# Kernel optimization log

Hardware: AMD Instinct MI355X
Metric: run time of the kernel (lower is better)

## Reference

```python
import jax, jax.numpy as jnp
import numpy as np
import math

B, S, E = 4, 4096, 1024
NUM_HEADS = 16
D = E // NUM_HEADS  # attention_size = 64


def setup_inputs() -> dict:
    key = jax.random.key(0)
    ks = jax.random.split(key, 7)
    queries = jax.random.normal(ks[0], (B, S, E), dtype=jnp.float32)
    keys = jax.random.normal(ks[1], (B, S, E), dtype=jnp.float32)
    values = jax.random.normal(ks[2], (B, S, E), dtype=jnp.float32)
    mask = jax.random.randint(ks[3], (B, S, S), 0, 2).astype(bool)
    # nn.Linear(E, D, bias=False): weight [D, E], y = x @ W^T
    lim = 1.0 / math.sqrt(E)
    W_q = jax.random.uniform(ks[4], (D, E), jnp.float32, -lim, lim)
    W_k = jax.random.uniform(ks[5], (D, E), jnp.float32, -lim, lim)
    W_v = jax.random.uniform(ks[6], (D, E), jnp.float32, -lim, lim)
    return {"queries": queries, "keys": keys, "values": values, "mask": mask,
            "W_q": W_q, "W_k": W_k, "W_v": W_v}


def reference(queries, keys, values, mask, W_q, W_k, W_v):
    Q = jnp.einsum('bse,de->bsd', queries, W_q)  # [B,S,D]
    K = jnp.einsum('bse,de->bsd', keys, W_k)
    V = jnp.einsum('bse,de->bsd', values, W_v)
    norm = math.sqrt(D)
    scores = jnp.einsum('bqd,bkd->bqk', Q, K) / norm  # [B,S,S]
    scores = jnp.where(mask, jnp.float32(-1e20), scores)
    attn = jax.nn.softmax(scores, axis=2)
    return jnp.einsum('bqk,bkd->bqd', attn, V)  # [B,S,D]
```

## Files before the change

### kernel.cpp

```cpp
#include <hip/hip_runtime.h>
#include <hip/hip_bf16.h>
#include <math.h>

#define NB 4
#define NS 4096
#define NE 1024
#define ND 64

typedef short bf16x8 __attribute__((ext_vector_type(8)));
typedef float f32x4  __attribute__((ext_vector_type(4)));

__device__ unsigned short g_Wb[3 * ND * NE];
__device__ unsigned short g_Qp[NB * NS * ND];
__device__ unsigned short g_Kp[NB * NS * ND];
__device__ unsigned short g_Vt[NB * ND * NS];
__device__ int g_flag;

static __device__ inline unsigned short f2bf(float f) {
    __hip_bfloat16 h = __float2bfloat16(f);
    return *reinterpret_cast<unsigned short*>(&h);
}
static __device__ inline unsigned int f2bf2(float lo, float hi) {
    __hip_bfloat162 h = __float22bfloat162_rn(make_float2(lo, hi));
    return *reinterpret_cast<unsigned int*>(&h);
}

static __device__ __forceinline__ void lds_fence() {
    asm volatile("s_waitcnt lgkmcnt(0)" ::: "memory");
    __builtin_amdgcn_sched_barrier(0);
}

__global__ void detect_mask(const unsigned int* __restrict__ mw) {
    __shared__ int found;
    if (threadIdx.x == 0) found = 0;
    __syncthreads();
    int f = 0;
    for (int i = threadIdx.x; i < 4096; i += 256)
        if (mw[i] > 1u) f = 1;
    if (f) atomicOr(&found, 1);
    __syncthreads();
    if (threadIdx.x == 0) g_flag = found;
}

__global__ void prep_w(const float* __restrict__ Wq, const float* __restrict__ Wk,
                       const float* __restrict__ Wv) {
    const int z = blockIdx.x;
    const float* W = (z == 0) ? Wq : (z == 1) ? Wk : Wv;
    unsigned short* o = g_Wb + (size_t)z * (ND * NE);
    const float scale = (z == 0) ? 0.125f : 1.0f;
    int i0 = blockIdx.y * 2048 + threadIdx.x * 8;
    float4 a = *(const float4*)&W[i0];
    float4 b = *(const float4*)&W[i0 + 4];
    ushort4 u0 = { f2bf(a.x * scale), f2bf(a.y * scale), f2bf(a.z * scale), f2bf(a.w * scale) };
    ushort4 u1 = { f2bf(b.x * scale), f2bf(b.y * scale), f2bf(b.z * scale), f2bf(b.w * scale) };
    *(ushort4*)&o[i0]     = u0;
    *(ushort4*)&o[i0 + 4] = u1;
}

__global__ __launch_bounds__(256) void proj_kernel(
    const float* __restrict__ Xq, const float* __restrict__ Xk, const float* __restrict__ Xv)
{
    __shared__ unsigned short Xs[2][64][72];

    const int z = blockIdx.y;
    const float* X = (z == 0) ? Xq : (z == 1) ? Xk : Xv;
    const unsigned short* W = g_Wb + (size_t)z * (ND * NE);

    const int t    = threadIdx.x;
    const int wv   = t >> 6;
    const int lane = t & 63;
    const int quad = lane >> 4;
    const int l16  = lane & 15;
    const int m0   = blockIdx.x * 64;

    const int sr  = t >> 4;
    const int sc4 = (t & 15) * 4;
    const float* Xb = X + (size_t)m0 * NE;

    float4 xv[4];

    #pragma unroll
    for (int p = 0; p < 4; ++p)
        xv[p] = *(const float4*)&Xb[(size_t)(sr + p * 16) * NE + sc4];
    #pragma unroll
    for (int p = 0; p < 4; ++p) {
        uint2 u = { f2bf2(xv[p].x, xv[p].y), f2bf2(xv[p].z, xv[p].w) };
        *(uint2*)&Xs[0][sr + p * 16][sc4] = u;
    }
    __syncthreads();

    f32x4 acc[4] = {};

    #pragma unroll 2
    for (int c = 0; c < 16; ++c) {
        const int buf = c & 1;
        const int e0  = c * 64;

        if (c < 15) {
            #pragma unroll
            for (int p = 0; p < 4; ++p)
                xv[p] = *(const float4*)&Xb[(size_t)(sr + p * 16) * NE + e0 + 64 + sc4];
        }

        #pragma unroll
        for (int ks = 0; ks < 2; ++ks) {
            bf16x8 a = *(const bf16x8*)&Xs[buf][wv * 16 + l16][ks * 32 + quad * 8];
            #pragma unroll
            for (int nt = 0; nt < 4; ++nt) {
                bf16x8 bb = *(const bf16x8*)&W[(size_t)(nt * 16 + l16) * NE + e0 + ks * 32 + quad * 8];
                acc[nt] = __builtin_amdgcn_mfma_f32_16x16x32_bf16(a, bb, acc[nt], 0, 0, 0);
            }
        }

        if (c < 15) {
            #pragma unroll
            for (int p = 0; p < 4; ++p) {
                uint2 u = { f2bf2(xv[p].x, xv[p].y), f2bf2(xv[p].z, xv[p].w) };
                *(uint2*)&Xs[buf ^ 1][sr + p * 16][sc4] = u;
            }
        }
        __syncthreads();
    }

    #pragma unroll
    for (int nt = 0; nt < 4; ++nt)
        #pragma unroll
        for (int r = 0; r < 4; ++r) {
            int m   = m0 + wv * 16 + quad * 4 + r;
            int col = nt * 16 + l16;
            unsigned short u = f2bf(acc[nt][r]);
            if (z == 0)      g_Qp[(size_t)m * ND + col] = u;
            else if (z == 1) g_Kp[(size_t)m * ND + col] = u;
            else             g_Vt[((size_t)(m >> 12) * ND + col) * NS + (m & 4095)] = u;
        }
}

__global__ __launch_bounds__(256) void attn_kernel(
    const void* __restrict__ maskp, float* __restrict__ out)
{
    __shared__ short Ss[4][2][16][72];
    __shared__ float Op[4][16][68];
    __shared__ float Lp[4][16];

    const int t    = threadIdx.x;
    const int wv   = t >> 6;
    const int lane = t & 63;
    const int quad = lane >> 4;
    const int l16  = lane & 15;
    const int b    = blockIdx.y;
    const int q0   = blockIdx.x * 16;
    const int koff = wv * 1024;

    const bool m_u8 = (g_flag != 0);
    const unsigned char* m8  = (const unsigned char*)maskp;
    const int*           m32 = (const int*)maskp;

    const unsigned short* Qrow = g_Qp + ((size_t)b * NS + q0 + l16) * ND;
    const bf16x8 qf0 = *(const bf16x8*)&Qrow[quad * 8];
    const bf16x8 qf1 = *(const bf16x8*)&Qrow[32 + quad * 8];

    const unsigned short* Kbase = g_Kp + ((size_t)b * NS) * ND;
    const unsigned short* Vbase = g_Vt + (size_t)b * ND * NS;

    float l_lane[4] = {};
    f32x4 Oacc[4] = {};

    #pragma unroll 2
    for (int it = 0; it < 16; ++it) {
        const int k0 = koff + it * 64;
        const int pb = it & 1;

        int mv[16];
        #pragma unroll
        for (int r = 0; r < 4; ++r) {
            size_t mrow = ((size_t)b * NS + (q0 + quad * 4 + r)) * (size_t)NS + k0;
            if (m_u8) {
                #pragma unroll
                for (int kt = 0; kt < 4; ++kt)
                    mv[kt * 4 + r] = (int)m8[mrow + kt * 16 + l16];
            } else {
                #pragma unroll
                for (int kt = 0; kt < 4; ++kt)
                    mv[kt * 4 + r] = m32[mrow + kt * 16 + l16];
            }
        }

        f32x4 sc[4] = {};
        __builtin_amdgcn_s_setprio(1);
        #pragma unroll
        for (int kt = 0; kt < 4; ++kt) {
            const unsigned short* Krow = Kbase + (size_t)(k0 + kt * 16 + l16) * ND;
            bf16x8 kf0 = *(const bf16x8*)&Krow[quad * 8];
            bf16x8 kf1 = *(const bf16x8*)&Krow[32 + quad * 8];
            sc[kt] = __builtin_amdgcn_mfma_f32_16x16x32_bf16(qf0, kf0, sc[kt], 0, 0, 0);
            sc[kt] = __builtin_amdgcn_mfma_f32_16x16x32_bf16(qf1, kf1, sc[kt], 0, 0, 0);
        }
        __builtin_amdgcn_s_setprio(0);

        bf16x8 vf[8];
        #pragma unroll
        for (int nt = 0; nt < 4; ++nt) {
            const unsigned short* Vrow = Vbase + (size_t)(nt * 16 + l16) * NS + k0;
            vf[2 * nt]     = *(const bf16x8*)&Vrow[quad * 8];
            vf[2 * nt + 1] = *(const bf16x8*)&Vrow[32 + quad * 8];
        }

        #pragma unroll
        for (int kt = 0; kt < 4; ++kt)
            #pragma unroll
            for (int r = 0; r < 4; ++r) {
                float p = mv[kt * 4 + r] ? 0.0f : __expf(sc[kt][r]);
                l_lane[r] += p;
                Ss[wv][pb][quad * 4 + r][kt * 16 + l16] = (short)f2bf(p);
            }

        lds_fence();

        bf16x8 a0 = *(const bf16x8*)&Ss[wv][pb][l16][quad * 8];
        bf16x8 a1 = *(const bf16x8*)&Ss[wv][pb][l16][32 + quad * 8];

        __builtin_amdgcn_s_setprio(1);
        #pragma unroll
        for (int nt = 0; nt < 4; ++nt) {
            Oacc[nt] = __builtin_amdgcn_mfma_f32_16x16x32_bf16(a0, vf[2 * nt],     Oacc[nt], 0, 0, 0);
            Oacc[nt] = __builtin_amdgcn_mfma_f32_16x16x32_bf16(a1, vf[2 * nt + 1], Oacc[nt], 0, 0, 0);
        }
        __builtin_amdgcn_s_setprio(0);
    }

    #pragma unroll
    for (int r = 0; r < 4; ++r) {
        #pragma unroll
        for (int off = 1; off < 16; off <<= 1)
            l_lane[r] += __shfl_xor(l_lane[r], off);
    }

    #pragma unroll
    for (int nt = 0; nt < 4; ++nt)
        #pragma unroll
        for (int r = 0; r < 4; ++r)
            Op[wv][quad * 4 + r][nt * 16 + l16] = Oacc[nt][r];
    if (l16 == 0) {
        #pragma unroll
        for (int r = 0; r < 4; ++r)
            Lp[wv][quad * 4 + r] = l_lane[r];
    }
    __syncthreads();

    {
        int q  = t >> 4;
        int d4 = (t & 15) * 4;
        f32x4 s = {};
        #pragma unroll
        for (int w = 0; w < 4; ++w)
            s += *(const f32x4*)&Op[w][q][d4];
        float l = Lp[0][q] + Lp[1][q] + Lp[2][q] + Lp[3][q];
        float inv = 1.0f / l;
        float4 o = { s[0] * inv, s[1] * inv, s[2] * inv, s[3] * inv };
        *(float4*)&out[((size_t)b * NS + q0 + q) * ND + d4] = o;
    }
}

extern "C" void kernel_launch(void* const* d_in, const int* in_sizes, int n_in,
                              void* d_out, int out_size, void* d_ws, size_t ws_size,
                              hipStream_t stream) {
    const float* queries = (const float*)d_in[0];
    const float* keys    = (const float*)d_in[1];
    const float* values  = (const float*)d_in[2];
    const void*  mask    = d_in[3];
    const float* Wq      = (const float*)d_in[4];
    const float* Wk      = (const float*)d_in[5];
    const float* Wv      = (const float*)d_in[6];
    float* out = (float*)d_out;

    hipLaunchKernelGGL(detect_mask, dim3(1), dim3(256), 0, stream,
                       (const unsigned int*)mask);
    hipLaunchKernelGGL(prep_w, dim3(3, 32), dim3(256), 0, stream, Wq, Wk, Wv);
    hipLaunchKernelGGL(proj_kernel, dim3((NB * NS) / 64, 3), dim3(256), 0, stream,
                       queries, keys, values);
    hipLaunchKernelGGL(attn_kernel, dim3(NS / 16, NB), dim3(256), 0, stream,
                       mask, out);
}
```

Before: 604.6 us.

## Stage mask tiles through LDS with vector loads and deepen projection prefetch

```diff
diff --git a/kernel.cpp b/kernel.cpp
--- a/kernel.cpp
+++ b/kernel.cpp
@@ -27,7 +27,6 @@
 
 static __device__ __forceinline__ void lds_fence() {
     asm volatile("s_waitcnt lgkmcnt(0)" ::: "memory");
-    __builtin_amdgcn_sched_barrier(0);
 }
 
 __global__ void detect_mask(const unsigned int* __restrict__ mw) {
@@ -77,46 +76,46 @@
     const int sc4 = (t & 15) * 4;
     const float* Xb = X + (size_t)m0 * NE;
 
-    float4 xv[4];
-
-    #pragma unroll
-    for (int p = 0; p < 4; ++p)
-        xv[p] = *(const float4*)&Xb[(size_t)(sr + p * 16) * NE + sc4];
+    float4 xr[4][4];
+
+    #pragma unroll
+    for (int d = 0; d < 4; ++d)
+        #pragma unroll
+        for (int p = 0; p < 4; ++p)
+            xr[d][p] = *(const float4*)&Xb[(size_t)(sr + p * 16) * NE + d * 64 + sc4];
     #pragma unroll
     for (int p = 0; p < 4; ++p) {
-        uint2 u = { f2bf2(xv[p].x, xv[p].y), f2bf2(xv[p].z, xv[p].w) };
+        uint2 u = { f2bf2(xr[0][p].x, xr[0][p].y), f2bf2(xr[0][p].z, xr[0][p].w) };
         *(uint2*)&Xs[0][sr + p * 16][sc4] = u;
     }
     __syncthreads();
 
     f32x4 acc[4] = {};
 
-    #pragma unroll 2
+    #pragma unroll
     for (int c = 0; c < 16; ++c) {
-        const int buf = c & 1;
-        const int e0  = c * 64;
-
-        if (c < 15) {
+        if (c + 4 < 16) {
             #pragma unroll
             for (int p = 0; p < 4; ++p)
-                xv[p] = *(const float4*)&Xb[(size_t)(sr + p * 16) * NE + e0 + 64 + sc4];
+                xr[c & 3][p] = *(const float4*)&Xb[(size_t)(sr + p * 16) * NE + (c + 4) * 64 + sc4];
         }
 
         #pragma unroll
         for (int ks = 0; ks < 2; ++ks) {
-            bf16x8 a = *(const bf16x8*)&Xs[buf][wv * 16 + l16][ks * 32 + quad * 8];
+            bf16x8 a = *(const bf16x8*)&Xs[c & 1][wv * 16 + l16][ks * 32 + quad * 8];
             #pragma unroll
             for (int nt = 0; nt < 4; ++nt) {
-                bf16x8 bb = *(const bf16x8*)&W[(size_t)(nt * 16 + l16) * NE + e0 + ks * 32 + quad * 8];
+                bf16x8 bb = *(const bf16x8*)&W[(size_t)(nt * 16 + l16) * NE + c * 64 + ks * 32 + quad * 8];
                 acc[nt] = __builtin_amdgcn_mfma_f32_16x16x32_bf16(a, bb, acc[nt], 0, 0, 0);
             }
         }
 
-        if (c < 15) {
+        if (c + 1 < 16) {
             #pragma unroll
             for (int p = 0; p < 4; ++p) {
-                uint2 u = { f2bf2(xv[p].x, xv[p].y), f2bf2(xv[p].z, xv[p].w) };
-                *(uint2*)&Xs[buf ^ 1][sr + p * 16][sc4] = u;
+                float4 v = xr[(c + 1) & 3][p];
+                uint2 u = { f2bf2(v.x, v.y), f2bf2(v.z, v.w) };
+                *(uint2*)&Xs[(c + 1) & 1][sr + p * 16][sc4] = u;
             }
         }
         __syncthreads();
@@ -135,12 +134,14 @@
         }
 }
 
-__global__ __launch_bounds__(256) void attn_kernel(
+__global__ __launch_bounds__(256, 4) void attn_kernel(
     const void* __restrict__ maskp, float* __restrict__ out)
 {
-    __shared__ short Ss[4][2][16][72];
-    __shared__ float Op[4][16][68];
-    __shared__ float Lp[4][16];
+    __shared__ __align__(16) char smem[28672];
+    short (*Ss)[2][16][72]         = reinterpret_cast<short(*)[2][16][72]>(smem);
+    unsigned char (*Mb)[2][16][80] = reinterpret_cast<unsigned char(*)[2][16][80]>(smem + 18432);
+    float (*Op)[16][68]            = reinterpret_cast<float(*)[16][68]>(smem);
+    float (*Lp)[16]                = reinterpret_cast<float(*)[16]>(smem + 17408);
 
     const int t    = threadIdx.x;
     const int wv   = t >> 6;
@@ -162,6 +163,15 @@
     const unsigned short* Kbase = g_Kp + ((size_t)b * NS) * ND;
     const unsigned short* Vbase = g_Vt + (size_t)b * ND * NS;
 
+    const int srow = lane >> 2;
+    const int scol = (lane & 3) * 16;
+    const unsigned char* m8row = m8 + ((size_t)b * NS + q0 + srow) * (size_t)NS + scol;
+
+    if (m_u8) {
+        uint4 mr0 = *(const uint4*)&m8row[koff];
+        *(uint4*)&Mb[wv][0][srow][scol] = mr0;
+    }
+
     float l_lane[4] = {};
     f32x4 Oacc[4] = {};
 
@@ -170,23 +180,7 @@
         const int k0 = koff + it * 64;
         const int pb = it & 1;
 
-        int mv[16];
-        #pragma unroll
-        for (int r = 0; r < 4; ++r) {
-            size_t mrow = ((size_t)b * NS + (q0 + quad * 4 + r)) * (size_t)NS + k0;
-            if (m_u8) {
-                #pragma unroll
-                for (int kt = 0; kt < 4; ++kt)
-                    mv[kt * 4 + r] = (int)m8[mrow + kt * 16 + l16];
-            } else {
-                #pragma unroll
-                for (int kt = 0; kt < 4; ++kt)
-                    mv[kt * 4 + r] = m32[mrow + kt * 16 + l16];
-            }
-        }
-
         f32x4 sc[4] = {};
-        __builtin_amdgcn_s_setprio(1);
         #pragma unroll
         for (int kt = 0; kt < 4; ++kt) {
             const unsigned short* Krow = Kbase + (size_t)(k0 + kt * 16 + l16) * ND;
@@ -195,7 +189,10 @@
             sc[kt] = __builtin_amdgcn_mfma_f32_16x16x32_bf16(qf0, kf0, sc[kt], 0, 0, 0);
             sc[kt] = __builtin_amdgcn_mfma_f32_16x16x32_bf16(qf1, kf1, sc[kt], 0, 0, 0);
         }
-        __builtin_amdgcn_s_setprio(0);
+
+        uint4 mr = {};
+        if (m_u8 && it < 15)
+            mr = *(const uint4*)&m8row[k0 + 64];
 
         bf16x8 vf[8];
         #pragma unroll
@@ -205,15 +202,35 @@
             vf[2 * nt + 1] = *(const bf16x8*)&Vrow[32 + quad * 8];
         }
 
+        int mvv[16];
+        if (m_u8) {
+            #pragma unroll
+            for (int kt = 0; kt < 4; ++kt)
+                #pragma unroll
+                for (int r = 0; r < 4; ++r)
+                    mvv[kt * 4 + r] = Mb[wv][pb][quad * 4 + r][kt * 16 + l16];
+        } else {
+            #pragma unroll
+            for (int r = 0; r < 4; ++r) {
+                size_t mrow = ((size_t)b * NS + (q0 + quad * 4 + r)) * (size_t)NS + k0;
+                #pragma unroll
+                for (int kt = 0; kt < 4; ++kt)
+                    mvv[kt * 4 + r] = m32[mrow + kt * 16 + l16];
+            }
+        }
+
         #pragma unroll
         for (int kt = 0; kt < 4; ++kt)
             #pragma unroll
             for (int r = 0; r < 4; ++r) {
-                float p = mv[kt * 4 + r] ? 0.0f : __expf(sc[kt][r]);
+                float p = mvv[kt * 4 + r] ? 0.0f : __expf(sc[kt][r]);
                 l_lane[r] += p;
                 Ss[wv][pb][quad * 4 + r][kt * 16 + l16] = (short)f2bf(p);
             }
 
+        if (m_u8 && it < 15)
+            *(uint4*)&Mb[wv][pb ^ 1][srow][scol] = mr;
+
         lds_fence();
 
         bf16x8 a0 = *(const bf16x8*)&Ss[wv][pb][l16][quad * 8];
@@ -227,6 +244,8 @@
         }
         __builtin_amdgcn_s_setprio(0);
     }
+
+    __syncthreads();
 
     #pragma unroll
     for (int r = 0; r < 4; ++r) {
```

Measured after the change: 607.2 us. About the same (+0.4%).
